# Kernel tuning notes

Hardware: AMD Instinct MI355X
Metric: run time of the kernel (lower is better)

Reference implementation:

```python
import jax, jax.numpy as jnp
from jax import lax
import numpy as np

B, N, C = 8, 32768, 256          # batch, num votes, seed_feat_dim
P, S = 256, 16                   # num_proposal, nsample
RADIUS = 0.3
NH, NS, NC = 1, 18, 18           # heading bins, size clusters, classes
OUT_DIM = 2 + 3 + NH * 2 + NS * 4 + NC  # 97
BN_EPS = 1e-3                    # keras BatchNormalization default epsilon
BN_SCALE = np.float32(1.0 / np.sqrt(1.0 + BN_EPS))  # moving_mean=0, moving_var=1
MEAN_SIZE = ((np.arange(NS * 3, dtype=np.float32).reshape(NS, 3) % 5.0) + 1.0) * 0.2


def _bn(x, g, b):
    # inference-mode BN with moving_mean=0, moving_var=1
    return g * (x * BN_SCALE) + b


def _fps(xyz, npoint):
    # farthest point sampling -> [B, npoint] int32 indices
    b, n = xyz.shape[0], xyz.shape[1]

    def step(carry, _):
        dist, last = carry                                   # [B,N], [B]
        p = jnp.take_along_axis(xyz, last[:, None, None], axis=1)  # [B,1,3]
        d = jnp.sum((xyz - p) ** 2, axis=-1)                 # [B,N]
        dist = jnp.minimum(dist, d)
        nxt = jnp.argmax(dist, axis=1).astype(jnp.int32)
        return (dist, nxt), last

    init = (jnp.full((b, n), 1e10, xyz.dtype), jnp.zeros((b,), jnp.int32))
    _, inds = lax.scan(step, init, None, length=npoint)
    return jnp.transpose(inds)                               # [B, npoint]


def _ball_query(xyz, new_xyz, radius, nsample):
    # first-nsample neighbors within radius, padded with first hit -> [B,P,S]
    n = xyz.shape[1]
    d2 = (jnp.sum(new_xyz ** 2, -1)[:, :, None]
          + jnp.sum(xyz ** 2, -1)[:, None, :]
          - 2.0 * jnp.einsum('bpd,bnd->bpn', new_xyz, xyz))  # [B,P,N]
    key = jnp.where(d2 < radius * radius, jnp.arange(n, dtype=jnp.int32), n)
    sel = -lax.top_k(-key, nsample)[0]                        # ascending smallest
    first = sel[..., :1]                                      # query point itself is always in-radius
    return jnp.where(sel < n, sel, first)


def _forward(xyz, features, mw0, mb0, mg0, me0, mw1, mb1, mg1, me1,
             mw2, mb2, mg2, me2, hw1, hb1, hg1, he1, hw2, hb2, hg2, he2, hw3, hb3):
    fps_inds = _fps(xyz, P)                                           # [B,P]
    new_xyz = jnp.take_along_axis(xyz, fps_inds[..., None], axis=1)   # [B,P,3]
    idx = _ball_query(xyz, new_xyz, RADIUS, S)                        # [B,P,S]

    g_xyz = jax.vmap(lambda pts, i: pts[i])(xyz, idx)                 # [B,P,S,3]
    g_xyz = (g_xyz - new_xyz[:, :, None, :]) / RADIUS                 # normalize_xyz
    g_feat = jax.vmap(lambda f, i: f[i])(features, idx)               # [B,P,S,C]
    h = jnp.concatenate([g_xyz, g_feat], axis=-1)                     # [B,P,S,C+3]

    # shared MLP (conv2d 1x1 + BN + ReLU) then max-pool over samples
    h = jax.nn.relu(_bn(h @ mw0 + mb0, mg0, me0))
    h = jax.nn.relu(_bn(h @ mw1 + mb1, mg1, me1))
    h = jax.nn.relu(_bn(h @ mw2 + mb2, mg2, me2))
    feats = jnp.max(h, axis=2)                                        # [B,P,128]

    # proposal head: conv1x1 + BN + ReLU x2, then conv1x1
    net = jax.nn.relu(_bn(feats @ hw1 + hb1, hg1, he1))
    net = jax.nn.relu(_bn(net @ hw2 + hb2, hg2, he2))
    net = net @ hw3 + hb3                                             # [B,P,97]

    # decode_scores
    obj = net[:, :, 0:2]
    center = new_xyz + net[:, :, 2:5]
    hs = net[:, :, 5:5 + NH]
    hrn = net[:, :, 5 + NH:5 + 2 * NH]
    hr = hrn * (np.pi / NH)
    ss = net[:, :, 5 + 2 * NH:5 + 2 * NH + NS]
    srn = net[:, :, 5 + 2 * NH + NS:5 + 2 * NH + 4 * NS].reshape(net.shape[0], P, NS, 3)
    sr = srn * jnp.asarray(MEAN_SIZE)[None, None]
    sem = net[:, :, 5 + 2 * NH + 4 * NS:]
    return (obj, center, hs, hrn, hr, ss, srn, sr, sem)


def setup_inputs() -> dict:
    key = jax.random.key(0)
    ks = jax.random.split(key, 16)

    def w(k, shape, scale=0.05):
        return jax.random.normal(k, shape, jnp.float32) * scale

    z, o = jnp.zeros, jnp.ones
    return {
        'xyz': jax.random.normal(ks[0], (B, N, 3), jnp.float32),
        'features': jax.random.normal(ks[1], (B, N, C), jnp.float32),
        'mw0': w(ks[2], (C + 3, 128)), 'mb0': z((128,)), 'mg0': o((128,)), 'me0': z((128,)),
        'mw1': w(ks[3], (128, 128)), 'mb1': z((128,)), 'mg1': o((128,)), 'me1': z((128,)),
        'mw2': w(ks[4], (128, 128)), 'mb2': z((128,)), 'mg2': o((128,)), 'me2': z((128,)),
        'hw1': w(ks[5], (128, 128)), 'hb1': z((128,)), 'hg1': o((128,)), 'he1': z((128,)),
        'hw2': w(ks[6], (128, 128)), 'hb2': z((128,)), 'hg2': o((128,)), 'he2': z((128,)),
        'hw3': w(ks[7], (128, OUT_DIM)), 'hb3': z((OUT_DIM,)),
    }


def reference(xyz, features, mw0, mb0, mg0, me0, mw1, mb1, mg1, me1,
              mw2, mb2, mg2, me2, hw1, hb1, hg1, he1, hw2, hb2, hg2, he2, hw3, hb3):
    return _forward(xyz, features, mw0, mb0, mg0, me0, mw1, mb1, mg1, me1,
                    mw2, mb2, mg2, me2, hw1, hb1, hg1, he1, hw2, hb2, hg2, he2, hw3, hb3)
```

## Files before the change

kernel.cpp:

```cpp
#include <hip/hip_runtime.h>
#include <math.h>

#define NBATCH 8
#define NPOINT 32768
#define NFEAT 256
#define NPROP 256
#define NSAMP 16
#define KIN 259
#define HDIM 128
#define ODIM 97

__device__ __forceinline__ float addrn(float a, float b) {
  float r; asm("v_add_f32 %0, %1, %2" : "=v"(r) : "v"(a), "v"(b)); return r;
}
__device__ __forceinline__ float subrn(float a, float b) {
  float r; asm("v_sub_f32 %0, %1, %2" : "=v"(r) : "v"(a), "v"(b)); return r;
}

__global__ __launch_bounds__(256)
void soa_kernel(const float* __restrict__ xyz, float* __restrict__ xs,
                float* __restrict__ ys, float* __restrict__ zs) {
  const int i = blockIdx.x * 256 + threadIdx.x;
  xs[i] = xyz[3*i+0];
  ys[i] = xyz[3*i+1];
  zs[i] = xyz[3*i+2];
}

#define FPS_DECL(g) float4 px##g, py##g, pz##g;
#define FPS_LOAD(g) \
  px##g = *(const float4*)&X[(g)*2048 + t4]; \
  py##g = *(const float4*)&Y[(g)*2048 + t4]; \
  pz##g = *(const float4*)&Z[(g)*2048 + t4]; \
  dist4[(g)*512 + t] = make_float4(1e10f, 1e10f, 1e10f, 1e10f);
#define FPS_UPD(c, g) { \
  const float dx = px##g.c - qx, dy = py##g.c - qy, dz = pz##g.c - qz; \
  const float d = addrn(addrn(dx*dx, dy*dy), dz*dz); \
  const float nd = fminf(dv.c, d); \
  dv.c = nd; \
  const bool gt = nd > bv_##c;                \
  bv_##c = gt ? nd : bv_##c; \
  bg_##c = gt ? (g) : bg_##c; }
#define FPS_STEP(g) { \
  float4 dv = dist4[(g)*512 + t]; \
  FPS_UPD(x, g) FPS_UPD(y, g) FPS_UPD(z, g) FPS_UPD(w, g) \
  dist4[(g)*512 + t] = dv; }

__global__ __launch_bounds__(512)
__attribute__((amdgpu_waves_per_eu(2, 2)))
void fps_kernel(const float* __restrict__ xs_, const float* __restrict__ ys_,
                const float* __restrict__ zs_, float* __restrict__ cxyz) {
  __shared__ __align__(16) float4 dist4[NPOINT/4];
  __shared__ float rv[8];
  __shared__ int ri[8];
  __shared__ int bc;
  const int b = blockIdx.x;
  const int t = threadIdx.x;
  const int t4 = t * 4;
  const float* __restrict__ X = xs_ + (size_t)b * NPOINT;
  const float* __restrict__ Y = ys_ + (size_t)b * NPOINT;
  const float* __restrict__ Z = zs_ + (size_t)b * NPOINT;
  FPS_DECL(0)  FPS_DECL(1)  FPS_DECL(2)  FPS_DECL(3)
  FPS_DECL(4)  FPS_DECL(5)  FPS_DECL(6)  FPS_DECL(7)
  FPS_DECL(8)  FPS_DECL(9)  FPS_DECL(10) FPS_DECL(11)
  FPS_DECL(12) FPS_DECL(13) FPS_DECL(14) FPS_DECL(15)
  FPS_LOAD(0)  FPS_LOAD(1)  FPS_LOAD(2)  FPS_LOAD(3)
  FPS_LOAD(4)  FPS_LOAD(5)  FPS_LOAD(6)  FPS_LOAD(7)
  FPS_LOAD(8)  FPS_LOAD(9)  FPS_LOAD(10) FPS_LOAD(11)
  FPS_LOAD(12) FPS_LOAD(13) FPS_LOAD(14) FPS_LOAD(15)
  __syncthreads();
  int last = 0;
  for (int step = 0; step < NPROP; ++step) {
    const float qx = X[last];
    const float qy = Y[last];
    const float qz = Z[last];
    if (t == 0) {
      cxyz[(b*NPROP+step)*3+0] = qx;
      cxyz[(b*NPROP+step)*3+1] = qy;
      cxyz[(b*NPROP+step)*3+2] = qz;
    }
    float bv_x = -1.0f, bv_y = -1.0f, bv_z = -1.0f, bv_w = -1.0f;
    int   bg_x = 0,     bg_y = 0,     bg_z = 0,     bg_w = 0;
    FPS_STEP(0)  FPS_STEP(1)  FPS_STEP(2)  FPS_STEP(3)
    FPS_STEP(4)  FPS_STEP(5)  FPS_STEP(6)  FPS_STEP(7)
    FPS_STEP(8)  FPS_STEP(9)  FPS_STEP(10) FPS_STEP(11)
    FPS_STEP(12) FPS_STEP(13) FPS_STEP(14) FPS_STEP(15)
    float bv = bv_x; int bi = bg_x*2048 + t4 + 0;
    { const int oi = bg_y*2048 + t4 + 1;
      if (bv_y > bv || (bv_y == bv && oi < bi)) { bv = bv_y; bi = oi; } }
    { const int oi = bg_z*2048 + t4 + 2;
      if (bv_z > bv || (bv_z == bv && oi < bi)) { bv = bv_z; bi = oi; } }
    { const int oi = bg_w*2048 + t4 + 3;
      if (bv_w > bv || (bv_w == bv && oi < bi)) { bv = bv_w; bi = oi; } }
#pragma unroll
    for (int m = 1; m < 64; m <<= 1) {
      const float ov = __shfl_xor(bv, m);
      const int   oi = __shfl_xor(bi, m);
      if (ov > bv || (ov == bv && oi < bi)) { bv = ov; bi = oi; }
    }
    if ((t & 63) == 0) { rv[t >> 6] = bv; ri[t >> 6] = bi; }
    __syncthreads();
    if (t < 64) {
      float fv = (t < 8) ? rv[t] : -2.0f;
      int   fi = (t < 8) ? ri[t] : 0x7fffffff;
#pragma unroll
      for (int m = 1; m < 8; m <<= 1) {
        const float ov = __shfl_xor(fv, m);
        const int   oi = __shfl_xor(fi, m);
        if (ov > fv || (ov == fv && oi < fi)) { fv = ov; fi = oi; }
      }
      if (t == 0) bc = fi;
    }
    __syncthreads();
    last = bc;
  }
}

__global__ __launch_bounds__(512)
void ballq_kernel(const float* __restrict__ xs_, const float* __restrict__ ys_,
                  const float* __restrict__ zs_, const float* __restrict__ cxyz,
                  int* __restrict__ idx) {
  const int gw = (blockIdx.x * 512 + threadIdx.x) >> 6;
  const int lane = threadIdx.x & 63;
  const int b = gw >> 8;
  const float* __restrict__ X = xs_ + (size_t)b * NPOINT;
  const float* __restrict__ Y = ys_ + (size_t)b * NPOINT;
  const float* __restrict__ Z = zs_ + (size_t)b * NPOINT;
  const float cx = cxyz[gw*3+0], cy = cxyz[gw*3+1], cz = cxyz[gw*3+2];
  const float a = addrn(addrn(cx*cx, cy*cy), cz*cz);
  const float R2 = (float)(0.3 * 0.3);
  int* __restrict__ out = idx + gw * NSAMP;
  int cnt = 0, first = -1;
  for (int base = 0; base < NPOINT; base += 64) {
    const int i = base + lane;
    const float x = X[i], y = Y[i], z = Z[i];
    const float bb2 = addrn(addrn(x*x, y*y), z*z);
    const float cc  = addrn(addrn(cx*x, cy*y), cz*z);
    const float d2  = subrn(addrn(a, bb2), 2.0f*cc);
    const bool isin = d2 < R2;
    const unsigned long long m = __ballot(isin);
    if (m) {
      if (first < 0) first = base + (int)__builtin_ctzll(m);
      if (isin) {
        const int pos = cnt + (int)__builtin_popcountll(m & ((1ull << lane) - 1ull));
        if (pos < NSAMP) out[pos] = i;
      }
      cnt += (int)__builtin_popcountll(m);
      if (cnt >= NSAMP) break;
    }
  }
  if (lane < NSAMP && lane >= cnt) out[lane] = first;
}

__global__ __launch_bounds__(256)
void mlp0_kernel(const float* __restrict__ xyz, const float* __restrict__ feat,
                 const float* __restrict__ cxyz, const int* __restrict__ idx,
                 const float* __restrict__ W, const float* __restrict__ bias_,
                 const float* __restrict__ gam_, const float* __restrict__ bet_,
                 float* __restrict__ h0) {
  __shared__ __align__(16) float w[KIN*132];
  __shared__ __align__(16) float xs[16*264];
  __shared__ int ids[16];
  const int t = threadIdx.x;
  for (int i = t; i < KIN*HDIM; i += 256) {
    const int k = i >> 7, c = i & 127;
    w[k*132 + c] = W[i];
  }
  const int r  = t >> 4;
  const int c8 = (t & 15) * 8;
  float bs[8], gm[8], bt[8];
#pragma unroll
  for (int j = 0; j < 8; ++j) { bs[j] = bias_[c8+j]; gm[j] = gam_[c8+j]; bt[j] = bet_[c8+j]; }
  const float bns = (float)(1.0 / sqrt(1.001));
  for (int gi = 0; gi < 8; ++gi) {
    const int g = blockIdx.x * 8 + gi;
    const int b = g >> 8;
    __syncthreads();
    if (t < 16) ids[t] = idx[g*16 + t];
    __syncthreads();
#pragma unroll
    for (int s = 0; s < 16; ++s)
      xs[s*264 + 3 + t] = feat[((size_t)b*NPOINT + ids[s])*NFEAT + t];
    if (t < 48) {
      const int s = t / 3, d = t - 3*(t/3);
      const float v = xyz[((size_t)b*NPOINT + ids[s])*3 + d];
      xs[s*264 + d] = (v - cxyz[g*3 + d]) / 0.3f;
    }
    __syncthreads();
    float acc[8];
#pragma unroll
    for (int j = 0; j < 8; ++j) acc[j] = bs[j];
    for (int k = 0; k < KIN; ++k) {
      const float xv = xs[r*264 + k];
      const float4 wa = *(const float4*)&w[k*132 + c8];
      const float4 wb = *(const float4*)&w[k*132 + c8 + 4];
      acc[0] += xv*wa.x; acc[1] += xv*wa.y; acc[2] += xv*wa.z; acc[3] += xv*wa.w;
      acc[4] += xv*wb.x; acc[5] += xv*wb.y; acc[6] += xv*wb.z; acc[7] += xv*wb.w;
    }
    float ov[8];
#pragma unroll
    for (int j = 0; j < 8; ++j) ov[j] = fmaxf(gm[j]*(acc[j]*bns)+bt[j], 0.0f);
    float* dst = &h0[((size_t)g*16 + r)*HDIM + c8];
    *(float4*)&dst[0] = make_float4(ov[0],ov[1],ov[2],ov[3]);
    *(float4*)&dst[4] = make_float4(ov[4],ov[5],ov[6],ov[7]);
  }
}

__global__ __launch_bounds__(256)
void mlp12_kernel(const float* __restrict__ h0,
                  const float* __restrict__ W1, const float* __restrict__ b1,
                  const float* __restrict__ g1, const float* __restrict__ e1,
                  const float* __restrict__ W2, const float* __restrict__ b2,
                  const float* __restrict__ g2, const float* __restrict__ e2,
                  float* __restrict__ feats) {
  __shared__ __align__(16) float w1[HDIM*132];
  __shared__ __align__(16) float w2[HDIM*132];
  __shared__ __align__(16) float xs[16*132];
  __shared__ __align__(16) float ys[16*132];
  const int t = threadIdx.x;
  for (int i = t; i < HDIM*HDIM; i += 256) {
    const int k = i >> 7, c = i & 127;
    w1[k*132+c] = W1[i];
    w2[k*132+c] = W2[i];
  }
  const int r  = t >> 4;
  const int c8 = (t & 15) * 8;
  float bs1[8], gm1[8], bt1[8], bs2[8], gm2[8], bt2[8];
#pragma unroll
  for (int j = 0; j < 8; ++j) {
    bs1[j]=b1[c8+j]; gm1[j]=g1[c8+j]; bt1[j]=e1[c8+j];
    bs2[j]=b2[c8+j]; gm2[j]=g2[c8+j]; bt2[j]=e2[c8+j];
  }
  const float bns = (float)(1.0 / sqrt(1.001));
  for (int gi = 0; gi < 8; ++gi) {
    const int g = blockIdx.x * 8 + gi;
    __syncthreads();
    for (int i = t; i < 16*HDIM; i += 256) {
      const int s = i >> 7, k = i & 127;
      xs[s*132+k] = h0[((size_t)g*16 + s)*HDIM + k];
    }
    __syncthreads();
    float acc[8];
#pragma unroll
    for (int j = 0; j < 8; ++j) acc[j] = bs1[j];
#pragma unroll 4
    for (int k = 0; k < HDIM; ++k) {
      const float xv = xs[r*132 + k];
      const float4 wa = *(const float4*)&w1[k*132 + c8];
      const float4 wb = *(const float4*)&w1[k*132 + c8 + 4];
      acc[0]+=xv*wa.x; acc[1]+=xv*wa.y; acc[2]+=xv*wa.z; acc[3]+=xv*wa.w;
      acc[4]+=xv*wb.x; acc[5]+=xv*wb.y; acc[6]+=xv*wb.z; acc[7]+=xv*wb.w;
    }
    {
      float ov[8];
#pragma unroll
      for (int j = 0; j < 8; ++j) ov[j] = fmaxf(gm1[j]*(acc[j]*bns)+bt1[j], 0.0f);
      *(float4*)&ys[r*132 + c8]     = make_float4(ov[0],ov[1],ov[2],ov[3]);
      *(float4*)&ys[r*132 + c8 + 4] = make_float4(ov[4],ov[5],ov[6],ov[7]);
    }
    __syncthreads();
#pragma unroll
    for (int j = 0; j < 8; ++j) acc[j] = bs2[j];
#pragma unroll 4
    for (int k = 0; k < HDIM; ++k) {
      const float xv = ys[r*132 + k];
      const float4 wa = *(const float4*)&w2[k*132 + c8];
      const float4 wb = *(const float4*)&w2[k*132 + c8 + 4];
      acc[0]+=xv*wa.x; acc[1]+=xv*wa.y; acc[2]+=xv*wa.z; acc[3]+=xv*wa.w;
      acc[4]+=xv*wb.x; acc[5]+=xv*wb.y; acc[6]+=xv*wb.z; acc[7]+=xv*wb.w;
    }
    {
      float ov[8];
#pragma unroll
      for (int j = 0; j < 8; ++j) ov[j] = fmaxf(gm2[j]*(acc[j]*bns)+bt2[j], 0.0f);
      *(float4*)&xs[r*132 + c8]     = make_float4(ov[0],ov[1],ov[2],ov[3]);
      *(float4*)&xs[r*132 + c8 + 4] = make_float4(ov[4],ov[5],ov[6],ov[7]);
    }
    __syncthreads();
#pragma unroll
    for (int hh = 8; hh >= 1; hh >>= 1) {
      if (r < hh) {
#pragma unroll
        for (int j = 0; j < 8; ++j)
          xs[r*132 + c8 + j] = fmaxf(xs[r*132 + c8 + j], xs[(r+hh)*132 + c8 + j]);
      }
      __syncthreads();
    }
    if (r == 0) {
      *(float4*)&feats[(size_t)g*HDIM + c8]     = *(float4*)&xs[c8];
      *(float4*)&feats[(size_t)g*HDIM + c8 + 4] = *(float4*)&xs[c8+4];
    }
  }
}

__global__ __launch_bounds__(256)
void head_kernel(const float* __restrict__ in_, const float* __restrict__ W,
                 const float* __restrict__ b_, const float* __restrict__ g_,
                 const float* __restrict__ e_, float* __restrict__ out_) {
  __shared__ __align__(16) float w[HDIM*132];
  __shared__ __align__(16) float xs[16*132];
  const int t = threadIdx.x;
  for (int i = t; i < HDIM*HDIM; i += 256) {
    const int k = i >> 7, c = i & 127;
    w[k*132+c] = W[i];
  }
  const int row0 = blockIdx.x * 16;
  for (int i = t; i < 16*HDIM; i += 256) {
    const int s = i >> 7, k = i & 127;
    xs[s*132+k] = in_[((size_t)row0 + s)*HDIM + k];
  }
  const int r  = t >> 4;
  const int c8 = (t & 15) * 8;
  float bs[8], gm[8], bt[8];
#pragma unroll
  for (int j = 0; j < 8; ++j) { bs[j]=b_[c8+j]; gm[j]=g_[c8+j]; bt[j]=e_[c8+j]; }
  const float bns = (float)(1.0 / sqrt(1.001));
  __syncthreads();
  float acc[8];
#pragma unroll
  for (int j = 0; j < 8; ++j) acc[j] = bs[j];
#pragma unroll 4
  for (int k = 0; k < HDIM; ++k) {
    const float xv = xs[r*132 + k];
    const float4 wa = *(const float4*)&w[k*132 + c8];
    const float4 wb = *(const float4*)&w[k*132 + c8 + 4];
    acc[0]+=xv*wa.x; acc[1]+=xv*wa.y; acc[2]+=xv*wa.z; acc[3]+=xv*wa.w;
    acc[4]+=xv*wb.x; acc[5]+=xv*wb.y; acc[6]+=xv*wb.z; acc[7]+=xv*wb.w;
  }
  float ov[8];
#pragma unroll
  for (int j = 0; j < 8; ++j) ov[j] = fmaxf(gm[j]*(acc[j]*bns)+bt[j], 0.0f);
  float* dst = &out_[((size_t)row0 + r)*HDIM + c8];
  *(float4*)&dst[0] = make_float4(ov[0],ov[1],ov[2],ov[3]);
  *(float4*)&dst[4] = make_float4(ov[4],ov[5],ov[6],ov[7]);
}

__global__ __launch_bounds__(128)
void head3_kernel(const float* __restrict__ net2, const float* __restrict__ W3,
                  const float* __restrict__ b3, const float* __restrict__ cxyz,
                  float* __restrict__ out) {
  __shared__ float x[HDIM];
  const int g = blockIdx.x;
  const int t = threadIdx.x;
  x[t] = net2[(size_t)g*HDIM + t];
  __syncthreads();
  if (t >= ODIM) return;
  float acc = b3[t];
#pragma unroll 4
  for (int k = 0; k < HDIM; ++k) acc += x[k] * W3[k*ODIM + t];
  const int OBJ=0, CEN=4096, HSo=10240, HRN=12288, HRo=14336,
            SSo=16384, SRN=53248, SRo=163840, SEM=274432;
  if (t < 2)       out[OBJ + g*2 + t] = acc;
  else if (t < 5)  out[CEN + g*3 + (t-2)] = acc + cxyz[g*3 + (t-2)];
  else if (t == 5) out[HSo + g] = acc;
  else if (t == 6) { out[HRN + g] = acc; out[HRo + g] = acc * (float)M_PI; }
  else if (t < 25) out[SSo + g*18 + (t-7)] = acc;
  else if (t < 79) {
    const int m2 = t - 25;
    out[SRN + g*54 + m2] = acc;
    out[SRo + g*54 + m2] = acc * ((float)(m2 % 5 + 1) * 0.2f);
  }
  else             out[SEM + g*18 + (t-79)] = acc;
}

extern "C" void kernel_launch(void* const* d_in, const int* in_sizes, int n_in,
                              void* d_out, int out_size, void* d_ws, size_t ws_size,
                              hipStream_t stream) {
  (void)in_sizes; (void)n_in; (void)out_size; (void)ws_size;
  const float* xyz  = (const float*)d_in[0];
  const float* feat = (const float*)d_in[1];
  const float* mw0 = (const float*)d_in[2];
  const float* mb0 = (const float*)d_in[3];
  const float* mg0 = (const float*)d_in[4];
  const float* me0 = (const float*)d_in[5];
  const float* mw1 = (const float*)d_in[6];
  const float* mb1 = (const float*)d_in[7];
  const float* mg1 = (const float*)d_in[8];
  const float* me1 = (const float*)d_in[9];
  const float* mw2 = (const float*)d_in[10];
  const float* mb2 = (const float*)d_in[11];
  const float* mg2 = (const float*)d_in[12];
  const float* me2 = (const float*)d_in[13];
  const float* hw1 = (const float*)d_in[14];
  const float* hb1 = (const float*)d_in[15];
  const float* hg1 = (const float*)d_in[16];
  const float* he1 = (const float*)d_in[17];
  const float* hw2 = (const float*)d_in[18];
  const float* hb2 = (const float*)d_in[19];
  const float* hg2 = (const float*)d_in[20];
  const float* he2 = (const float*)d_in[21];
  const float* hw3 = (const float*)d_in[22];
  const float* hb3 = (const float*)d_in[23];
  float* out = (float*)d_out;
  char* ws = (char*)d_ws;
  float* cxyz = (float*)(ws + 8192);
  int*   idx  = (int*)(ws + 32768);
  float* h0   = (float*)(ws + 163840);
  float* xs   = (float*)(ws + 163840);
  float* ys   = (float*)(ws + 163840 + 1048576);
  float* zs   = (float*)(ws + 163840 + 2097152);
  float* fts  = (float*)(ws + 16941056);
  float* net1 = (float*)(ws + 17989632);
  float* net2 = (float*)(ws + 19038208);

  soa_kernel<<<1024, 256, 0, stream>>>(xyz, xs, ys, zs);
  fps_kernel<<<NBATCH, 512, 0, stream>>>(xs, ys, zs, cxyz);
  ballq_kernel<<<256, 512, 0, stream>>>(xs, ys, zs, cxyz, idx);
  mlp0_kernel<<<256, 256, 0, stream>>>(xyz, feat, cxyz, idx, mw0, mb0, mg0, me0, h0);
  mlp12_kernel<<<256, 256, 0, stream>>>(h0, mw1, mb1, mg1, me1, mw2, mb2, mg2, me2, fts);
  head_kernel<<<128, 256, 0, stream>>>(fts, hw1, hb1, hg1, he1, net1);
  head_kernel<<<128, 256, 0, stream>>>(net1, hw2, hb2, hg2, he2, net2);
  head3_kernel<<<2048, 128, 0, stream>>>(net2, hw3, hb3, cxyz, out);
}
```

Before: 1.438 ms.

## Keep part of FPS points in registers and stream the rest double-buffered

The FPS kernel no longer holds all 16 float4 groups of xyz in registers. It keeps 6 groups resident and reloads the other 10 from global memory (L2) every step, using a two-slot software pipeline so each load is issued one group ahead of its use. The waves_per_eu(2,2) attribute is dropped, which lowers register pressure and may allow more waves per SIMD. The cost is roughly 30 extra global loads per thread per step across 256 sequential steps, with load latency on the critical serial path.

```diff
diff --git a/kernel.cpp b/kernel.cpp
--- a/kernel.cpp
+++ b/kernel.cpp
@@ -26,27 +26,41 @@
   zs[i] = xyz[3*i+2];
 }
 
-#define FPS_DECL(g) float4 px##g, py##g, pz##g;
-#define FPS_LOAD(g) \
-  px##g = *(const float4*)&X[(g)*2048 + t4]; \
-  py##g = *(const float4*)&Y[(g)*2048 + t4]; \
-  pz##g = *(const float4*)&Z[(g)*2048 + t4]; \
-  dist4[(g)*512 + t] = make_float4(1e10f, 1e10f, 1e10f, 1e10f);
-#define FPS_UPD(c, g) { \
-  const float dx = px##g.c - qx, dy = py##g.c - qy, dz = pz##g.c - qz; \
-  const float d = addrn(addrn(dx*dx, dy*dy), dz*dz); \
+#define FPS_RDECL(g) float4 px##g, py##g, pz##g;
+#define FPS_RLOAD(g) \
+  px##g = X4[(g)*512 + t]; \
+  py##g = Y4[(g)*512 + t]; \
+  pz##g = Z4[(g)*512 + t]; \
+  dist4[(g)*512 + t] = q10;
+#define FPS_SINIT(g) dist4[(g)*512 + t] = q10;
+#define FPS_UPDC(c, g, SX, SY, SZ) { \
+  const float dx = SX.c - qx, dy = SY.c - qy, dz = SZ.c - qz; \
+  const float d = addrn(addrn(dx*dx, dy*dy), dz*dz);   \
   const float nd = fminf(dv.c, d); \
   dv.c = nd; \
   const bool gt = nd > bv_##c;                \
   bv_##c = gt ? nd : bv_##c; \
   bg_##c = gt ? (g) : bg_##c; }
-#define FPS_STEP(g) { \
+#define FPS_STEP_R(g) { \
   float4 dv = dist4[(g)*512 + t]; \
-  FPS_UPD(x, g) FPS_UPD(y, g) FPS_UPD(z, g) FPS_UPD(w, g) \
+  FPS_UPDC(x, g, px##g, py##g, pz##g) \
+  FPS_UPDC(y, g, px##g, py##g, pz##g) \
+  FPS_UPDC(z, g, px##g, py##g, pz##g) \
+  FPS_UPDC(w, g, px##g, py##g, pz##g) \
   dist4[(g)*512 + t] = dv; }
+#define FPS_ISSUE(B, g) \
+  B##x = X4[(g)*512 + t]; \
+  B##y = Y4[(g)*512 + t]; \
+  B##z = Z4[(g)*512 + t];
+#define FPS_STEP_S(B, g) { \
+  float4 dv = dist4[(g)*512 + t]; \
+  FPS_UPDC(x, g, B##x, B##y, B##z) \
+  FPS_UPDC(y, g, B##x, B##y, B##z) \
+  FPS_UPDC(z, g, B##x, B##y, B##z) \
+  FPS_UPDC(w, g, B##x, B##y, B##z) \
+  dist4[(g)*512 + t] = dv; }
 
 __global__ __launch_bounds__(512)
-__attribute__((amdgpu_waves_per_eu(2, 2)))
 void fps_kernel(const float* __restrict__ xs_, const float* __restrict__ ys_,
                 const float* __restrict__ zs_, float* __restrict__ cxyz) {
   __shared__ __align__(16) float4 dist4[NPOINT/4];
@@ -59,14 +73,16 @@
   const float* __restrict__ X = xs_ + (size_t)b * NPOINT;
   const float* __restrict__ Y = ys_ + (size_t)b * NPOINT;
   const float* __restrict__ Z = zs_ + (size_t)b * NPOINT;
-  FPS_DECL(0)  FPS_DECL(1)  FPS_DECL(2)  FPS_DECL(3)
-  FPS_DECL(4)  FPS_DECL(5)  FPS_DECL(6)  FPS_DECL(7)
-  FPS_DECL(8)  FPS_DECL(9)  FPS_DECL(10) FPS_DECL(11)
-  FPS_DECL(12) FPS_DECL(13) FPS_DECL(14) FPS_DECL(15)
-  FPS_LOAD(0)  FPS_LOAD(1)  FPS_LOAD(2)  FPS_LOAD(3)
-  FPS_LOAD(4)  FPS_LOAD(5)  FPS_LOAD(6)  FPS_LOAD(7)
-  FPS_LOAD(8)  FPS_LOAD(9)  FPS_LOAD(10) FPS_LOAD(11)
-  FPS_LOAD(12) FPS_LOAD(13) FPS_LOAD(14) FPS_LOAD(15)
+  const float4* __restrict__ X4 = (const float4*)X;
+  const float4* __restrict__ Y4 = (const float4*)Y;
+  const float4* __restrict__ Z4 = (const float4*)Z;
+  const float4 q10 = make_float4(1e10f, 1e10f, 1e10f, 1e10f);
+  FPS_RDECL(0) FPS_RDECL(1) FPS_RDECL(2) FPS_RDECL(3) FPS_RDECL(4) FPS_RDECL(5)
+  float4 sAx, sAy, sAz, sBx, sBy, sBz;
+  FPS_RLOAD(0) FPS_RLOAD(1) FPS_RLOAD(2) FPS_RLOAD(3) FPS_RLOAD(4) FPS_RLOAD(5)
+  FPS_SINIT(6)  FPS_SINIT(7)  FPS_SINIT(8)  FPS_SINIT(9)
+  FPS_SINIT(10) FPS_SINIT(11) FPS_SINIT(12) FPS_SINIT(13)
+  FPS_SINIT(14) FPS_SINIT(15)
   __syncthreads();
   int last = 0;
   for (int step = 0; step < NPROP; ++step) {
@@ -80,10 +96,19 @@
     }
     float bv_x = -1.0f, bv_y = -1.0f, bv_z = -1.0f, bv_w = -1.0f;
     int   bg_x = 0,     bg_y = 0,     bg_z = 0,     bg_w = 0;
-    FPS_STEP(0)  FPS_STEP(1)  FPS_STEP(2)  FPS_STEP(3)
-    FPS_STEP(4)  FPS_STEP(5)  FPS_STEP(6)  FPS_STEP(7)
-    FPS_STEP(8)  FPS_STEP(9)  FPS_STEP(10) FPS_STEP(11)
-    FPS_STEP(12) FPS_STEP(13) FPS_STEP(14) FPS_STEP(15)
+    FPS_ISSUE(sA, 6)
+    FPS_STEP_R(0) FPS_STEP_R(1) FPS_STEP_R(2)
+    FPS_STEP_R(3) FPS_STEP_R(4) FPS_STEP_R(5)
+    FPS_ISSUE(sB, 7)  FPS_STEP_S(sA, 6)
+    FPS_ISSUE(sA, 8)  FPS_STEP_S(sB, 7)
+    FPS_ISSUE(sB, 9)  FPS_STEP_S(sA, 8)
+    FPS_ISSUE(sA, 10) FPS_STEP_S(sB, 9)
+    FPS_ISSUE(sB, 11) FPS_STEP_S(sA, 10)
+    FPS_ISSUE(sA, 12) FPS_STEP_S(sB, 11)
+    FPS_ISSUE(sB, 13) FPS_STEP_S(sA, 12)
+    FPS_ISSUE(sA, 14) FPS_STEP_S(sB, 13)
+    FPS_ISSUE(sB, 15) FPS_STEP_S(sA, 14)
+    FPS_STEP_S(sB, 15)
     float bv = bv_x; int bi = bg_x*2048 + t4 + 0;
     { const int oi = bg_y*2048 + t4 + 1;
       if (bv_y > bv || (bv_y == bv && oi < bi)) { bv = bv_y; bi = oi; } }
```

Result: no change. 1.437 ms (-0.1%).

## Split farthest point sampling across four blocks per batch with a global atomic barrier

Applied to the files above, without the earlier changes.

The FPS kernel now launches four blocks per batch, each keeping an 8192-point chunk in registers and LDS instead of one block owning all 32768 points. After each step, every block publishes its best value and index as one packed 64-bit atomicMax. It then spins on a per-batch counter until all four chunks have reported, and reads the winning point. This spreads the serial 256-step loop over four times as many CUs, at the cost of a global atomic handshake with spin-waiting on every step. It also relies on all 32 blocks being resident at once; if they are not, the spin-wait deadlocks.

```diff
diff --git a/kernel.cpp b/kernel.cpp
--- a/kernel.cpp
+++ b/kernel.cpp
@@ -9,6 +9,8 @@
 #define KIN 259
 #define HDIM 128
 #define ODIM 97
+#define NCHUNK 4
+#define CHSZ 8192
 
 __device__ __forceinline__ float addrn(float a, float b) {
   float r; asm("v_add_f32 %0, %1, %2" : "=v"(r) : "v"(a), "v"(b)); return r;
@@ -19,22 +21,31 @@
 
 __global__ __launch_bounds__(256)
 void soa_kernel(const float* __restrict__ xyz, float* __restrict__ xs,
-                float* __restrict__ ys, float* __restrict__ zs) {
+                float* __restrict__ ys, float* __restrict__ zs,
+                unsigned int* __restrict__ cnt,
+                unsigned long long* __restrict__ slots) {
   const int i = blockIdx.x * 256 + threadIdx.x;
   xs[i] = xyz[3*i+0];
   ys[i] = xyz[3*i+1];
   zs[i] = xyz[3*i+2];
+  if (i < NBATCH) cnt[i] = 0u;
+  if (i < NBATCH*NPROP) slots[i] = 0ull;
+}
+
+__device__ __forceinline__ unsigned long long packvi(float v, unsigned gi) {
+  return ((unsigned long long)__float_as_uint(v) << 32) |
+         (unsigned long long)(0xFFFFFFFFu - gi);
 }
 
 #define FPS_DECL(g) float4 px##g, py##g, pz##g;
 #define FPS_LOAD(g) \
-  px##g = *(const float4*)&X[(g)*2048 + t4]; \
-  py##g = *(const float4*)&Y[(g)*2048 + t4]; \
-  pz##g = *(const float4*)&Z[(g)*2048 + t4]; \
+  px##g = X4[(g)*512 + t]; \
+  py##g = Y4[(g)*512 + t]; \
+  pz##g = Z4[(g)*512 + t]; \
   dist4[(g)*512 + t] = make_float4(1e10f, 1e10f, 1e10f, 1e10f);
 #define FPS_UPD(c, g) { \
   const float dx = px##g.c - qx, dy = py##g.c - qy, dz = pz##g.c - qz; \
-  const float d = addrn(addrn(dx*dx, dy*dy), dz*dz); \
+  const float d = addrn(addrn(dx*dx, dy*dy), dz*dz);   \
   const float nd = fminf(dv.c, d); \
   dv.c = nd; \
   const bool gt = nd > bv_##c;                \
@@ -46,44 +57,42 @@
   dist4[(g)*512 + t] = dv; }
 
 __global__ __launch_bounds__(512)
-__attribute__((amdgpu_waves_per_eu(2, 2)))
 void fps_kernel(const float* __restrict__ xs_, const float* __restrict__ ys_,
-                const float* __restrict__ zs_, float* __restrict__ cxyz) {
-  __shared__ __align__(16) float4 dist4[NPOINT/4];
+                const float* __restrict__ zs_, float* __restrict__ cxyz,
+                unsigned int* __restrict__ cnt,
+                unsigned long long* __restrict__ slots) {
+  __shared__ __align__(16) float4 dist4[CHSZ/4];
   __shared__ float rv[8];
   __shared__ int ri[8];
-  __shared__ int bc;
-  const int b = blockIdx.x;
+  __shared__ float qsh[3];
+  const int batch = blockIdx.x & 7;
+  const int chunk = blockIdx.x >> 3;
   const int t = threadIdx.x;
   const int t4 = t * 4;
-  const float* __restrict__ X = xs_ + (size_t)b * NPOINT;
-  const float* __restrict__ Y = ys_ + (size_t)b * NPOINT;
-  const float* __restrict__ Z = zs_ + (size_t)b * NPOINT;
-  FPS_DECL(0)  FPS_DECL(1)  FPS_DECL(2)  FPS_DECL(3)
-  FPS_DECL(4)  FPS_DECL(5)  FPS_DECL(6)  FPS_DECL(7)
-  FPS_DECL(8)  FPS_DECL(9)  FPS_DECL(10) FPS_DECL(11)
-  FPS_DECL(12) FPS_DECL(13) FPS_DECL(14) FPS_DECL(15)
-  FPS_LOAD(0)  FPS_LOAD(1)  FPS_LOAD(2)  FPS_LOAD(3)
-  FPS_LOAD(4)  FPS_LOAD(5)  FPS_LOAD(6)  FPS_LOAD(7)
-  FPS_LOAD(8)  FPS_LOAD(9)  FPS_LOAD(10) FPS_LOAD(11)
-  FPS_LOAD(12) FPS_LOAD(13) FPS_LOAD(14) FPS_LOAD(15)
+  const float* __restrict__ X = xs_ + (size_t)batch * NPOINT;
+  const float* __restrict__ Y = ys_ + (size_t)batch * NPOINT;
+  const float* __restrict__ Z = zs_ + (size_t)batch * NPOINT;
+  const float4* __restrict__ X4 = (const float4*)(X + chunk * CHSZ);
+  const float4* __restrict__ Y4 = (const float4*)(Y + chunk * CHSZ);
+  const float4* __restrict__ Z4 = (const float4*)(Z + chunk * CHSZ);
+  unsigned int* __restrict__ cnt_p = cnt + batch;
+  unsigned long long* __restrict__ slot_p = slots + batch * NPROP;
+  FPS_DECL(0) FPS_DECL(1) FPS_DECL(2) FPS_DECL(3)
+  FPS_LOAD(0) FPS_LOAD(1) FPS_LOAD(2) FPS_LOAD(3)
+  if (t == 0) { qsh[0] = X[0]; qsh[1] = Y[0]; qsh[2] = Z[0]; }
   __syncthreads();
-  int last = 0;
   for (int step = 0; step < NPROP; ++step) {
-    const float qx = X[last];
-    const float qy = Y[last];
-    const float qz = Z[last];
-    if (t == 0) {
-      cxyz[(b*NPROP+step)*3+0] = qx;
-      cxyz[(b*NPROP+step)*3+1] = qy;
-      cxyz[(b*NPROP+step)*3+2] = qz;
+    const float qx = qsh[0];
+    const float qy = qsh[1];
+    const float qz = qsh[2];
+    if (t == 0 && chunk == 0) {
+      cxyz[(batch*NPROP+step)*3+0] = qx;
+      cxyz[(batch*NPROP+step)*3+1] = qy;
+      cxyz[(batch*NPROP+step)*3+2] = qz;
     }
     float bv_x = -1.0f, bv_y = -1.0f, bv_z = -1.0f, bv_w = -1.0f;
     int   bg_x = 0,     bg_y = 0,     bg_z = 0,     bg_w = 0;
-    FPS_STEP(0)  FPS_STEP(1)  FPS_STEP(2)  FPS_STEP(3)
-    FPS_STEP(4)  FPS_STEP(5)  FPS_STEP(6)  FPS_STEP(7)
-    FPS_STEP(8)  FPS_STEP(9)  FPS_STEP(10) FPS_STEP(11)
-    FPS_STEP(12) FPS_STEP(13) FPS_STEP(14) FPS_STEP(15)
+    FPS_STEP(0) FPS_STEP(1) FPS_STEP(2) FPS_STEP(3)
     float bv = bv_x; int bi = bg_x*2048 + t4 + 0;
     { const int oi = bg_y*2048 + t4 + 1;
       if (bv_y > bv || (bv_y == bv && oi < bi)) { bv = bv_y; bi = oi; } }
@@ -108,10 +117,23 @@
         const int   oi = __shfl_xor(fi, m);
         if (ov > fv || (ov == fv && oi < fi)) { fv = ov; fi = oi; }
       }
-      if (t == 0) bc = fi;
-    }
-    __syncthreads();
-    last = bc;
+      if (t == 0) {
+        const unsigned gi = (unsigned)(chunk * CHSZ + fi);
+        atomicMax(slot_p + step, packvi(fv, gi));
+        __hip_atomic_fetch_add(cnt_p, 1u, __ATOMIC_RELEASE,
+                               __HIP_MEMORY_SCOPE_AGENT);
+        const unsigned target = 4u * (unsigned)(step + 1);
+        while (__hip_atomic_load(cnt_p, __ATOMIC_ACQUIRE,
+                                 __HIP_MEMORY_SCOPE_AGENT) < target)
+          __builtin_amdgcn_s_sleep(8);
+        const unsigned long long w =
+            __hip_atomic_load(slot_p + step, __ATOMIC_ACQUIRE,
+                              __HIP_MEMORY_SCOPE_AGENT);
+        const int gw = (int)(0xFFFFFFFFu - (unsigned)(w & 0xFFFFFFFFull));
+        qsh[0] = X[gw]; qsh[1] = Y[gw]; qsh[2] = Z[gw];
+      }
+    }
+    __syncthreads();
   }
 }
 
@@ -394,6 +416,8 @@
   char* ws = (char*)d_ws;
   float* cxyz = (float*)(ws + 8192);
   int*   idx  = (int*)(ws + 32768);
+  unsigned int*       cnt   = (unsigned int*)(ws + 32768);
+  unsigned long long* slots = (unsigned long long*)(ws + 32832);
   float* h0   = (float*)(ws + 163840);
   float* xs   = (float*)(ws + 163840);
   float* ys   = (float*)(ws + 163840 + 1048576);
@@ -402,8 +426,8 @@
   float* net1 = (float*)(ws + 17989632);
   float* net2 = (float*)(ws + 19038208);
 
-  soa_kernel<<<1024, 256, 0, stream>>>(xyz, xs, ys, zs);
-  fps_kernel<<<NBATCH, 512, 0, stream>>>(xs, ys, zs, cxyz);
+  soa_kernel<<<1024, 256, 0, stream>>>(xyz, xs, ys, zs, cnt, slots);
+  fps_kernel<<<NBATCH * NCHUNK, 512, 0, stream>>>(xs, ys, zs, cxyz, cnt, slots);
   ballq_kernel<<<256, 512, 0, stream>>>(xs, ys, zs, cxyz, idx);
   mlp0_kernel<<<256, 256, 0, stream>>>(xyz, feat, cxyz, idx, mw0, mb0, mg0, me0, h0);
   mlp12_kernel<<<256, 256, 0, stream>>>(h0, mw1, mb1, mg1, me1, mw2, mb2, mg2, me2, fts);
```

Result: faster. 1.310 ms (-8.9%).
